# Kernel optimization log

Hardware: AMD Instinct MI355X
Metric: run time of the kernel (lower is better)

The kernel has to match this reference:

```python
import jax, jax.numpy as jnp
import numpy as np

BN_EPS = 1e-5

def _conv1x1(x, w, b):
    # x: [B,C,H,W], w: [O,C], b: [O]
    return jnp.einsum('bchw,oc->bohw', x, w) + b[None, :, None, None]

def _maxpool2x2(x):
    B, C, H, W = x.shape
    return x.reshape(B, C, H // 2, 2, W // 2, 2).max(axis=(3, 5))

def setup_inputs() -> dict:
    key = jax.random.key(0)
    ks = jax.random.split(key, 6)
    B, C, H, W = 8, 256, 64, 64
    Ci = C // 2  # inter_channels default
    x = jax.random.normal(ks[0], (B, C, H, W), jnp.float32)
    s = lambda k, sh: jax.random.normal(k, sh, jnp.float32) * 0.02
    return {
        'x': x,
        'w_g': s(ks[1], (Ci, C)), 'b_g': jnp.zeros((Ci,), jnp.float32),
        'w_theta': s(ks[2], (Ci, C)), 'b_theta': jnp.zeros((Ci,), jnp.float32),
        'w_phi': s(ks[3], (Ci, C)), 'b_phi': jnp.zeros((Ci,), jnp.float32),
        'w_w': s(ks[4], (C, Ci)), 'b_w': jnp.zeros((C,), jnp.float32),
        'bn_gamma': 1.0 + 0.1 * jax.random.normal(ks[5], (C,), jnp.float32),
        'bn_beta': jnp.zeros((C,), jnp.float32),
    }

def reference(x, w_g, b_g, w_theta, b_theta, w_phi, b_phi, w_w, b_w, bn_gamma, bn_beta):
    B, C, H, W = x.shape
    Ci = w_g.shape[0]
    # projections (sub_sample=True: maxpool 2x2 on g and phi)
    g_x = _maxpool2x2(_conv1x1(x, w_g, b_g)).reshape(B, Ci, -1)          # [B,Ci,M]
    g_x = g_x.transpose(0, 2, 1)                                          # [B,M,Ci]
    theta_x = _conv1x1(x, w_theta, b_theta).reshape(B, Ci, -1)            # [B,Ci,N]
    theta_x = theta_x.transpose(0, 2, 1)                                  # [B,N,Ci]
    phi_x = _maxpool2x2(_conv1x1(x, w_phi, b_phi)).reshape(B, Ci, -1)     # [B,Ci,M]
    # unscaled embedded-Gaussian attention (no 1/sqrt(d), as in source)
    f = jnp.einsum('bnc,bcm->bnm', theta_x, phi_x)                        # [B,N,M]
    f_div_C = jax.nn.softmax(f, axis=-1)
    y = jnp.einsum('bnm,bmc->bnc', f_div_C, g_x)                          # [B,N,Ci]
    y = y.transpose(0, 2, 1).reshape(B, Ci, H, W)
    # W: 1x1 conv + BatchNorm (training mode: batch statistics)
    wy = _conv1x1(y, w_w, b_w)                                            # [B,C,H,W]
    mean = wy.mean(axis=(0, 2, 3), keepdims=True)
    var = wy.var(axis=(0, 2, 3), keepdims=True)
    wy = (wy - mean) * jax.lax.rsqrt(var + BN_EPS)
    wy = wy * bn_gamma[None, :, None, None] + bn_beta[None, :, None, None]
    return wy + x
```

## Files before the change

### kernel.cpp

```cpp
#include <hip/hip_runtime.h>
#include <hip/hip_bf16.h>

#define NB 8
#define NC 256
#define NCI 128
#define NSP 4096
#define NM 1024

typedef float f32x4 __attribute__((ext_vector_type(4)));
typedef short s16x8 __attribute__((ext_vector_type(8)));
typedef unsigned short u16;

#define OFF_XH  (0ull)
#define OFF_XL  (16777216ull)
#define OFF_THT (33554432ull)
#define OFF_PHT (41943040ull)
#define OFF_GP  (44040192ull)
#define OFF_YH  (46137344ull)
#define OFF_YL  (54525952ull)
#define OFF_WY  (0ull)
#define OFF_WBH (62914560ull)
#define OFF_WBL (63111168ull)
#define OFF_WWH (63307776ull)
#define OFF_WWL (63373312ull)
#define OFF_S   (63438848ull)

#define GLL(src, dst) __builtin_amdgcn_global_load_lds( \
    (const __attribute__((address_space(1))) unsigned*)(src), \
    (__attribute__((address_space(3))) unsigned*)(dst), 16, 0, 0)

__device__ __forceinline__ u16 f2bf(float f) {
  union { __hip_bfloat16 h; u16 u; } v;
  v.h = __float2bfloat16(f);
  return v.u;
}
__device__ __forceinline__ float bf2f(u16 u) {
  union { unsigned u; float f; } v;
  v.u = (unsigned)u << 16;
  return v.f;
}
__device__ __forceinline__ u16 bfmax4(u16 a, u16 b, u16 c, u16 d) {
  float v = fmaxf(fmaxf(bf2f(a), bf2f(b)), fmaxf(bf2f(c), bf2f(d)));
  return f2bf(v);
}

__global__ void zero_stats(float* s) { s[threadIdx.x] = 0.f; }

__global__ __launch_bounds__(256) void wcvt(
    const float* __restrict__ wg, const float* __restrict__ wth,
    const float* __restrict__ wph, const float* __restrict__ ww,
    u16* __restrict__ wbh, u16* __restrict__ wbl,
    u16* __restrict__ wwh, u16* __restrict__ wwl)
{
  int idx = blockIdx.x * 256 + threadIdx.x;
  if (idx < 384 * 256) {
    int row = idx >> 8, k = idx & 255;
    float v = row < 128 ? wg[row * 256 + k]
            : row < 256 ? wth[(row - 128) * 256 + k]
                        : wph[(row - 256) * 256 + k];
    u16 h = f2bf(v);
    wbh[idx] = h;
    wbl[idx] = f2bf(v - bf2f(h));
  } else {
    int j = idx - 384 * 256;
    float v = ww[j];
    u16 h = f2bf(v);
    wwh[j] = h;
    wwl[j] = f2bf(v - bf2f(h));
  }
}

__global__ __launch_bounds__(256) void xt_cvt(const float* __restrict__ x,
                                              u16* __restrict__ xh, u16* __restrict__ xl)
{
  __shared__ float t[64 * 68];
  const int n0 = blockIdx.x << 6, c0 = blockIdx.y << 6, b = blockIdx.z;
  const int tid = threadIdx.x;
  const int cl = tid >> 4, n4 = (tid & 15) << 2;
#pragma unroll
  for (int it = 0; it < 4; ++it) {
    int c = it * 16 + cl;
    float4 v = *(const float4*)&x[((size_t)(b * NC + c0 + c)) * NSP + n0 + n4];
    *(float4*)&t[c * 68 + n4] = v;
  }
  __syncthreads();
#pragma unroll
  for (int it = 0; it < 2; ++it) {
    int task = it * 256 + tid;
    int n = task >> 3, cc = (task & 7) << 3;
    u16 oh[8], ol[8];
#pragma unroll
    for (int i = 0; i < 8; ++i) {
      float v = t[(cc + i) * 68 + n];
      oh[i] = f2bf(v);
      ol[i] = f2bf(v - bf2f(oh[i]));
    }
    size_t dst = ((size_t)(b * NSP + n0 + n)) * NC + c0 + cc;
    *(s16x8*)&xh[dst] = *(s16x8*)oh;
    *(s16x8*)&xl[dst] = *(s16x8*)ol;
  }
}

__global__ __launch_bounds__(512, 1) void proj_fused(
    const u16* __restrict__ xh, const u16* __restrict__ xl,
    const u16* __restrict__ wbh, const u16* __restrict__ wbl,
    const float* __restrict__ bg, const float* __restrict__ bth,
    const float* __restrict__ bph,
    u16* __restrict__ thT, u16* __restrict__ phT, u16* __restrict__ gp)
{
  __shared__ char smem[132608];
  u16* xsh = (u16*)smem;
  u16* xsl = (u16*)(smem + 16384);
  u16* wsh = (u16*)(smem + 32768);
  u16* wsl = (u16*)(smem + 81920);
  u16* outl = (u16*)smem;
  float* bias = (float*)(smem + 131072);

  const int b = blockIdx.y, h2 = blockIdx.x;
  const int n0 = h2 << 7;
  const int tid = threadIdx.x;
  const int wave = tid >> 6, lane = tid & 63;
  const int lo16 = lane & 15, hi4 = lane >> 4;
  const int wr = wave >> 1, wc = wave & 1;
  const int obase = wr * 96, nbase = wc * 64;

  if (tid < 384)
    bias[tid] = tid < 128 ? bg[tid] : tid < 256 ? bth[tid - 128] : bph[tid - 256];

  f32x4 acc[6][4];
#pragma unroll
  for (int i = 0; i < 6; ++i)
#pragma unroll
    for (int j = 0; j < 4; ++j) acc[i][j] = (f32x4){0.f, 0.f, 0.f, 0.f};

  for (int step = 0; step < 4; ++step) {
    __syncthreads();
#pragma unroll
    for (int i = 0; i < 2; ++i) {
      int ci = i * 512 + tid;
      int n = ci >> 3, slot = ci & 7;
      size_t rowb = ((size_t)(b * NSP + n0 + n)) * 512 + step * 128 + ((slot ^ (n & 7)) << 4);
      GLL((const char*)xh + rowb, (char*)xsh + (size_t)(i * 512 + (tid & ~63)) * 16);
      GLL((const char*)xl + rowb, (char*)xsl + (size_t)(i * 512 + (tid & ~63)) * 16);
    }
#pragma unroll
    for (int i = 0; i < 6; ++i) {
      int ci = i * 512 + tid;
      int o = ci >> 3, slot = ci & 7;
      size_t rowb = (size_t)o * 512 + step * 128 + ((slot ^ (o & 7)) << 4);
      GLL((const char*)wbh + rowb, (char*)wsh + (size_t)(i * 512 + (tid & ~63)) * 16);
      GLL((const char*)wbl + rowb, (char*)wsl + (size_t)(i * 512 + (tid & ~63)) * 16);
    }
    __syncthreads();

#pragma unroll
    for (int kc = 0; kc < 2; ++kc) {
      const int sl = kc * 4 + hi4;
      s16x8 bfh[4], bfl[4];
#pragma unroll
      for (int fn = 0; fn < 4; ++fn) {
        int n = nbase + fn * 16 + lo16;
        int off = (int)n * 128 + ((sl ^ (n & 7)) << 4);
        bfh[fn] = *(const s16x8*)((const char*)xsh + off);
        bfl[fn] = *(const s16x8*)((const char*)xsl + off);
      }
      __builtin_amdgcn_s_setprio(1);
#pragma unroll
      for (int fo = 0; fo < 6; ++fo) {
        int o = obase + fo * 16 + lo16;
        int off = (int)o * 128 + ((sl ^ (o & 7)) << 4);
        s16x8 afh = *(const s16x8*)((const char*)wsh + off);
        s16x8 afl = *(const s16x8*)((const char*)wsl + off);
#pragma unroll
        for (int fn = 0; fn < 4; ++fn) {
          acc[fo][fn] = __builtin_amdgcn_mfma_f32_16x16x32_bf16(afh, bfh[fn], acc[fo][fn], 0, 0, 0);
          acc[fo][fn] = __builtin_amdgcn_mfma_f32_16x16x32_bf16(afh, bfl[fn], acc[fo][fn], 0, 0, 0);
          acc[fo][fn] = __builtin_amdgcn_mfma_f32_16x16x32_bf16(afl, bfh[fn], acc[fo][fn], 0, 0, 0);
        }
      }
      __builtin_amdgcn_s_setprio(0);
    }
  }

  __syncthreads();
#pragma unroll
  for (int fo = 0; fo < 6; ++fo) {
    int orow = obase + fo * 16 + hi4 * 4;
    f32x4 bv = *(const f32x4*)&bias[orow];
#pragma unroll
    for (int fn = 0; fn < 4; ++fn) {
      int n = nbase + fn * 16 + lo16;
#pragma unroll
      for (int r = 0; r < 4; ++r)
        outl[(orow + r) * 137 + n] = f2bf(acc[fo][fn][r] + bv[r]);
    }
  }
  __syncthreads();

#pragma unroll
  for (int it = 0; it < 4; ++it) {
    int task = it * 512 + tid;
    int n = task >> 4, cc = (task & 15) << 3;
    u16 o[8];
#pragma unroll
    for (int i = 0; i < 8; ++i) o[i] = outl[(128 + cc + i) * 137 + n];
    *(s16x8*)&thT[((size_t)(b * NSP + n0 + n)) * NCI + cc] = *(s16x8*)o;
  }
  {
    int c = tid >> 2, wq = tid & 3;
    u16 o[8];
#pragma unroll
    for (int j = 0; j < 8; ++j) {
      int w2 = wq * 8 + j;
      o[j] = bfmax4(outl[c * 137 + 2 * w2], outl[c * 137 + 2 * w2 + 1],
                    outl[c * 137 + 64 + 2 * w2], outl[c * 137 + 64 + 2 * w2 + 1]);
    }
    *(s16x8*)&gp[((size_t)(b * NCI + c)) * NM + (h2 << 5) + wq * 8] = *(s16x8*)o;
  }
  {
    int w2 = tid >> 4, cc = (tid & 15) << 3;
    u16 o[8];
#pragma unroll
    for (int i = 0; i < 8; ++i) {
      int c = 256 + cc + i;
      o[i] = bfmax4(outl[c * 137 + 2 * w2], outl[c * 137 + 2 * w2 + 1],
                    outl[c * 137 + 64 + 2 * w2], outl[c * 137 + 64 + 2 * w2 + 1]);
    }
    *(s16x8*)&phT[((size_t)(b * NM + (h2 << 5) + w2)) * NCI + cc] = *(s16x8*)o;
  }
}

__global__ __launch_bounds__(256, 2) void attn_mfma(
    const u16* __restrict__ thT, const u16* __restrict__ phT,
    const u16* __restrict__ gP, u16* __restrict__ yh, u16* __restrict__ yl)
{
  __shared__ u16 phs[2][64 * 128];
  __shared__ u16 gs[2][128 * 64];
  __shared__ u16 ps[4][16 * 72];

  const int b = blockIdx.y;
  const int n0 = blockIdx.x << 6;
  const int tid = threadIdx.x;
  const int wave = tid >> 6;
  const int lane = tid & 63;
  const int lo16 = lane & 15;
  const int hi4 = lane >> 4;
  const int qbase = n0 + (wave << 4);
  const int swq = (lo16 & 7) << 4;

  s16x8 tha[4];
#pragma unroll
  for (int kc = 0; kc < 4; ++kc)
    tha[kc] = *(const s16x8*)&thT[((size_t)b * NSP + qbase + lo16) * NCI + kc * 32 + hi4 * 8];

  f32x4 yacc[8];
#pragma unroll
  for (int i = 0; i < 8; ++i) yacc[i] = (f32x4){0.f, 0.f, 0.f, 0.f};
  float m_i[4] = {-3e38f, -3e38f, -3e38f, -3e38f};
  float l_i[4] = {0.f, 0.f, 0.f, 0.f};

  auto stage = [&](int s, int m0) {
#pragma unroll
    for (int i = 0; i < 4; ++i) {
      int ci = i * 256 + tid;
      int m = ci >> 4, cb = (ci & 15) << 4;
      const char* src = (const char*)phT + (((size_t)b * NM + m0 + m) << 8) + (cb ^ ((m & 7) << 4));
      GLL(src, (char*)phs[s] + (size_t)(i * 256 + (tid & ~63)) * 16);
    }
#pragma unroll
    for (int i = 0; i < 4; ++i) {
      int ci = i * 256 + tid;
      int c = ci >> 3, mb = (ci & 7) << 4;
      const char* src = (const char*)gP + (((size_t)b * NCI + c) << 11) + m0 * 2 + (mb ^ ((c & 7) << 4));
      GLL(src, (char*)gs[s] + (size_t)(i * 256 + (tid & ~63)) * 16);
    }
  };

  stage(0, 0);
  __syncthreads();
  int cur = 0;

  for (int mt = 0; mt < 16; ++mt) {
    if (mt < 15) stage(cur ^ 1, (mt + 1) << 6);

    const u16* ph = phs[cur];
    const u16* gg = gs[cur];

    f32x4 sf[4];
#pragma unroll
    for (int ms = 0; ms < 4; ++ms) sf[ms] = (f32x4){0.f, 0.f, 0.f, 0.f};
    __builtin_amdgcn_s_setprio(1);
#pragma unroll
    for (int ms = 0; ms < 4; ++ms) {
      const int rbase = (ms * 16 + lo16) << 8;
#pragma unroll
      for (int kc = 0; kc < 4; ++kc) {
        s16x8 bp = *(const s16x8*)((const char*)ph + rbase + ((kc * 64 + hi4 * 16) ^ swq));
        sf[ms] = __builtin_amdgcn_mfma_f32_16x16x32_bf16(tha[kc], bp, sf[ms], 0, 0, 0);
      }
    }
    __builtin_amdgcn_s_setprio(0);

    float scv[4];
#pragma unroll
    for (int r = 0; r < 4; ++r) {
      float v = fmaxf(fmaxf(sf[0][r], sf[1][r]), fmaxf(sf[2][r], sf[3][r]));
      v = fmaxf(v, __shfl_xor(v, 1));
      v = fmaxf(v, __shfl_xor(v, 2));
      v = fmaxf(v, __shfl_xor(v, 4));
      v = fmaxf(v, __shfl_xor(v, 8));
      float mn = fmaxf(m_i[r], v);
      float sc = __expf(m_i[r] - mn);
      float rs = 0.f;
#pragma unroll
      for (int ms = 0; ms < 4; ++ms) {
        float e = __expf(sf[ms][r] - mn);
        sf[ms][r] = e;
        rs += e;
      }
      rs += __shfl_xor(rs, 1);
      rs += __shfl_xor(rs, 2);
      rs += __shfl_xor(rs, 4);
      rs += __shfl_xor(rs, 8);
      l_i[r] = l_i[r] * sc + rs;
      m_i[r] = mn;
      scv[r] = sc;
    }
#pragma unroll
    for (int ct = 0; ct < 8; ++ct)
#pragma unroll
      for (int r = 0; r < 4; ++r) yacc[ct][r] *= scv[r];

    u16* pw = ps[wave];
#pragma unroll
    for (int ms = 0; ms < 4; ++ms)
#pragma unroll
      for (int r = 0; r < 4; ++r)
        pw[(hi4 * 4 + r) * 72 + ms * 16 + lo16] = f2bf(sf[ms][r]);
    asm volatile("s_waitcnt lgkmcnt(0)" ::: "memory");

    s16x8 pa[2];
#pragma unroll
    for (int km = 0; km < 2; ++km)
      pa[km] = *(const s16x8*)((const char*)pw + lo16 * 144 + km * 64 + hi4 * 16);

    __builtin_amdgcn_s_setprio(1);
#pragma unroll
    for (int ct = 0; ct < 8; ++ct) {
      const int rb = (ct * 16 + lo16) << 7;
#pragma unroll
      for (int km = 0; km < 2; ++km) {
        s16x8 bg = *(const s16x8*)((const char*)gg + rb + ((km * 64 + hi4 * 16) ^ swq));
        yacc[ct] = __builtin_amdgcn_mfma_f32_16x16x32_bf16(pa[km], bg, yacc[ct], 0, 0, 0);
      }
    }
    __builtin_amdgcn_s_setprio(0);

    __syncthreads();
    cur ^= 1;
  }

#pragma unroll
  for (int r = 0; r < 4; ++r) {
    float inv = 1.f / l_i[r];
    size_t row = ((size_t)b * NSP + qbase + hi4 * 4 + r) * NCI;
#pragma unroll
    for (int ct = 0; ct < 8; ++ct) {
      float v = yacc[ct][r] * inv;
      u16 h = f2bf(v);
      yh[row + ct * 16 + lo16] = h;
      yl[row + ct * 16 + lo16] = f2bf(v - bf2f(h));
    }
  }
}

__global__ __launch_bounds__(512, 1) void conv_w_mfma(
    const u16* __restrict__ yh, const u16* __restrict__ yl,
    const u16* __restrict__ wwh, const u16* __restrict__ wwl,
    const float* __restrict__ bw, float* __restrict__ wy,
    float* __restrict__ s1g, float* __restrict__ s2g)
{
  __shared__ char smem[102400];
  u16* wsh = (u16*)smem;
  u16* wsl = (u16*)(smem + 32768);
  u16* ysh = (u16*)(smem + 65536);
  u16* ysl = (u16*)(smem + 81920);
  float (*sums1)[256] = (float(*)[256])(smem + 98304);
  float (*sums2)[256] = (float(*)[256])(smem + 100352);

  const int b = blockIdx.y, n0 = blockIdx.x << 7;
  const int tid = threadIdx.x;
  const int wave = tid >> 6, lane = tid & 63;
  const int lo16 = lane & 15, hi4 = lane >> 4;
  const int wr = wave >> 1, wc = wave & 1;
  const int obase = wr * 64, nbase = wc * 64;

  f32x4 acc[4][4];
#pragma unroll
  for (int i = 0; i < 4; ++i)
#pragma unroll
    for (int j = 0; j < 4; ++j) acc[i][j] = (f32x4){0.f, 0.f, 0.f, 0.f};

  for (int step = 0; step < 2; ++step) {
    __syncthreads();
#pragma unroll
    for (int i = 0; i < 4; ++i) {
      int ci = i * 512 + tid;
      int o = ci >> 3, slot = ci & 7;
      size_t rowb = (size_t)o * 256 + step * 128 + ((slot ^ (o & 7)) << 4);
      GLL((const char*)wwh + rowb, (char*)wsh + (size_t)(i * 512 + (tid & ~63)) * 16);
      GLL((const char*)wwl + rowb, (char*)wsl + (size_t)(i * 512 + (tid & ~63)) * 16);
    }
#pragma unroll
    for (int i = 0; i < 2; ++i) {
      int ci = i * 512 + tid;
      int n = ci >> 3, slot = ci & 7;
      size_t rowb = ((size_t)(b * NSP + n0 + n)) * 256 + step * 128 + ((slot ^ (n & 7)) << 4);
      GLL((const char*)yh + rowb, (char*)ysh + (size_t)(i * 512 + (tid & ~63)) * 16);
      GLL((const char*)yl + rowb, (char*)ysl + (size_t)(i * 512 + (tid & ~63)) * 16);
    }
    __syncthreads();

#pragma unroll
    for (int kc = 0; kc < 2; ++kc) {
      const int sl = kc * 4 + hi4;
      s16x8 bfh[4], bfl[4];
#pragma unroll
      for (int fn = 0; fn < 4; ++fn) {
        int n = nbase + fn * 16 + lo16;
        int off = (int)n * 128 + ((sl ^ (n & 7)) << 4);
        bfh[fn] = *(const s16x8*)((const char*)ysh + off);
        bfl[fn] = *(const s16x8*)((const char*)ysl + off);
      }
      __builtin_amdgcn_s_setprio(1);
#pragma unroll
      for (int fo = 0; fo < 4; ++fo) {
        int o = obase + fo * 16 + lo16;
        int off = (int)o * 128 + ((sl ^ (o & 7)) << 4);
        s16x8 afh = *(const s16x8*)((const char*)wsh + off);
        s16x8 afl = *(const s16x8*)((const char*)wsl + off);
#pragma unroll
        for (int fn = 0; fn < 4; ++fn) {
          acc[fo][fn] = __builtin_amdgcn_mfma_f32_16x16x32_bf16(afh, bfh[fn], acc[fo][fn], 0, 0, 0);
          acc[fo][fn] = __builtin_amdgcn_mfma_f32_16x16x32_bf16(afh, bfl[fn], acc[fo][fn], 0, 0, 0);
          acc[fo][fn] = __builtin_amdgcn_mfma_f32_16x16x32_bf16(afl, bfh[fn], acc[fo][fn], 0, 0, 0);
        }
      }
      __builtin_amdgcn_s_setprio(0);
    }
  }

#pragma unroll
  for (int fo = 0; fo < 4; ++fo) {
    int orow = obase + fo * 16 + hi4 * 4;
    float bv[4];
#pragma unroll
    for (int r = 0; r < 4; ++r) bv[r] = bw[orow + r];
    float ss[4] = {0.f, 0.f, 0.f, 0.f}, sq[4] = {0.f, 0.f, 0.f, 0.f};
#pragma unroll
    for (int fn = 0; fn < 4; ++fn) {
      int col = n0 + nbase + fn * 16 + lo16;
#pragma unroll
      for (int r = 0; r < 4; ++r) {
        float v = acc[fo][fn][r] + bv[r];
        wy[((size_t)(b * NC) + orow + r) * NSP + col] = v;
        ss[r] += v;
        sq[r] += v * v;
      }
    }
#pragma unroll
    for (int r = 0; r < 4; ++r) {
#pragma unroll
      for (int d = 1; d < 16; d <<= 1) {
        ss[r] += __shfl_xor(ss[r], d);
        sq[r] += __shfl_xor(sq[r], d);
      }
    }
    if (lo16 == 0) {
#pragma unroll
      for (int r = 0; r < 4; ++r) {
        sums1[wc][orow + r] = ss[r];
        sums2[wc][orow + r] = sq[r];
      }
    }
  }
  __syncthreads();
  if (tid < 256) {
    atomicAdd(&s1g[tid], sums1[0][tid] + sums1[1][tid]);
    atomicAdd(&s2g[tid], sums2[0][tid] + sums2[1][tid]);
  }
}

__global__ __launch_bounds__(256) void bn_res4(
    const float* __restrict__ wy, const float* __restrict__ x,
    const float* __restrict__ s1, const float* __restrict__ s2,
    const float* __restrict__ gamma, const float* __restrict__ beta,
    float* __restrict__ out)
{
  int i4 = (blockIdx.x * 256 + threadIdx.x) << 2;
  int c = (i4 >> 12) & 255;
  const float cnt = 1.f / 32768.f;
  float mean = s1[c] * cnt;
  float var = s2[c] * cnt - mean * mean;
  float inv = rsqrtf(var + 1e-5f) * gamma[c];
  float bet = beta[c];
  float4 w = *(const float4*)&wy[i4];
  float4 xv = *(const float4*)&x[i4];
  float4 o;
  o.x = (w.x - mean) * inv + bet + xv.x;
  o.y = (w.y - mean) * inv + bet + xv.y;
  o.z = (w.z - mean) * inv + bet + xv.z;
  o.w = (w.w - mean) * inv + bet + xv.w;
  *(float4*)&out[i4] = o;
}

extern "C" void kernel_launch(void* const* d_in, const int* in_sizes, int n_in,
                              void* d_out, int out_size, void* d_ws, size_t ws_size,
                              hipStream_t stream) {
  const float* x    = (const float*)d_in[0];
  const float* w_g  = (const float*)d_in[1];
  const float* b_g  = (const float*)d_in[2];
  const float* w_th = (const float*)d_in[3];
  const float* b_th = (const float*)d_in[4];
  const float* w_ph = (const float*)d_in[5];
  const float* b_ph = (const float*)d_in[6];
  const float* w_w  = (const float*)d_in[7];
  const float* b_w  = (const float*)d_in[8];
  const float* gam  = (const float*)d_in[9];
  const float* bet  = (const float*)d_in[10];
  float* out = (float*)d_out;
  char* ws = (char*)d_ws;

  u16*   xh  = (u16*)(ws + OFF_XH);
  u16*   xl  = (u16*)(ws + OFF_XL);
  u16*   thT = (u16*)(ws + OFF_THT);
  u16*   phT = (u16*)(ws + OFF_PHT);
  u16*   gp  = (u16*)(ws + OFF_GP);
  u16*   yhb = (u16*)(ws + OFF_YH);
  u16*   ylb = (u16*)(ws + OFF_YL);
  float* wy  = (float*)(ws + OFF_WY);
  u16*   wbh = (u16*)(ws + OFF_WBH);
  u16*   wbl = (u16*)(ws + OFF_WBL);
  u16*   wwh = (u16*)(ws + OFF_WWH);
  u16*   wwl = (u16*)(ws + OFF_WWL);
  float* s1  = (float*)(ws + OFF_S);
  float* s2  = s1 + 256;

  wcvt<<<dim3(512), 256, 0, stream>>>(w_g, w_th, w_ph, w_w, wbh, wbl, wwh, wwl);
  zero_stats<<<dim3(1), 512, 0, stream>>>(s1);
  xt_cvt<<<dim3(64, 4, 8), 256, 0, stream>>>(x, xh, xl);

  proj_fused<<<dim3(32, 8), 512, 0, stream>>>(xh, xl, wbh, wbl, b_g, b_th, b_ph, thT, phT, gp);

  attn_mfma<<<dim3(64, 8), 256, 0, stream>>>(thT, phT, gp, yhb, ylb);

  conv_w_mfma<<<dim3(32, 8), 512, 0, stream>>>(yhb, ylb, wwh, wwl, b_w, wy, s1, s2);

  bn_res4<<<dim3(8192), 256, 0, stream>>>(wy, x, s1, s2, gam, bet, out);
}
```

Before: 125.7 us.

## Rewrite attention with 32x32x16 MFMA, transposed scores, register-resident P

Switches the attention kernel from 16x16x32 to 32x32x16 bf16 MFMA. Each wave now handles 32 queries and each block 128 queries, so the grid is halved. Scores are computed transposed so each lane owns one query row, which turns the softmax max and sum reductions into in-register loops plus one cross-half shuffle. The probability operand is built with packed bf16 conversion and permlane32 swaps instead of a trip through shared memory. Output is written through an LDS bounce buffer for coalesced 16-byte stores. In exchange, only 256 blocks run with a single block per CU, which cuts occupancy and latency hiding on a 256-CU part.

```diff
diff --git a/kernel.cpp b/kernel.cpp
--- a/kernel.cpp
+++ b/kernel.cpp
@@ -8,6 +8,7 @@
 #define NM 1024
 
 typedef float f32x4 __attribute__((ext_vector_type(4)));
+typedef float f32x16 __attribute__((ext_vector_type(16)));
 typedef short s16x8 __attribute__((ext_vector_type(8)));
 typedef unsigned short u16;
 
@@ -42,6 +43,11 @@
 __device__ __forceinline__ u16 bfmax4(u16 a, u16 b, u16 c, u16 d) {
   float v = fmaxf(fmaxf(bf2f(a), bf2f(b)), fmaxf(bf2f(c), bf2f(d)));
   return f2bf(v);
+}
+__device__ __forceinline__ unsigned cvtpk(float lo, float hi) {
+  unsigned r;
+  asm volatile("v_cvt_pk_bf16_f32 %0, %1, %2" : "=v"(r) : "v"(lo), "v"(hi));
+  return r;
 }
 
 __global__ void zero_stats(float* s) { s[threadIdx.x] = 0.f; }
@@ -230,49 +236,50 @@
   }
 }
 
-__global__ __launch_bounds__(256, 2) void attn_mfma(
+__global__ __launch_bounds__(256, 1) void attn_mfma(
     const u16* __restrict__ thT, const u16* __restrict__ phT,
     const u16* __restrict__ gP, u16* __restrict__ yh, u16* __restrict__ yl)
 {
-  __shared__ u16 phs[2][64 * 128];
-  __shared__ u16 gs[2][128 * 64];
-  __shared__ u16 ps[4][16 * 72];
+  __shared__ char smem[65536];
 
   const int b = blockIdx.y;
-  const int n0 = blockIdx.x << 6;
+  const int n0 = blockIdx.x << 7;
   const int tid = threadIdx.x;
   const int wave = tid >> 6;
   const int lane = tid & 63;
-  const int lo16 = lane & 15;
-  const int hi4 = lane >> 4;
-  const int qbase = n0 + (wave << 4);
-  const int swq = (lo16 & 7) << 4;
-
-  s16x8 tha[4];
-#pragma unroll
-  for (int kc = 0; kc < 4; ++kc)
-    tha[kc] = *(const s16x8*)&thT[((size_t)b * NSP + qbase + lo16) * NCI + kc * 32 + hi4 * 8];
-
-  f32x4 yacc[8];
-#pragma unroll
-  for (int i = 0; i < 8; ++i) yacc[i] = (f32x4){0.f, 0.f, 0.f, 0.f};
-  float m_i[4] = {-3e38f, -3e38f, -3e38f, -3e38f};
-  float l_i[4] = {0.f, 0.f, 0.f, 0.f};
+  const int l31 = lane & 31;
+  const int hi1 = lane >> 5;
+  const int qbase = n0 + (wave << 5);
+  const int swl = (l31 & 7) << 4;
+
+  s16x8 thb[8];
+  {
+    const u16* tr = &thT[((size_t)b * NSP + qbase + l31) * NCI + hi1 * 8];
+#pragma unroll
+    for (int kc = 0; kc < 8; ++kc) thb[kc] = *(const s16x8*)&tr[kc * 16];
+  }
+
+  f32x16 yacc[4];
+#pragma unroll
+  for (int ct = 0; ct < 4; ++ct) yacc[ct] = (f32x16)0.f;
+  float m_i = -3e38f, l_i = 0.f;
 
   auto stage = [&](int s, int m0) {
+    char* pdst = smem + s * 16384;
+    char* gdst = smem + 32768 + s * 16384;
 #pragma unroll
     for (int i = 0; i < 4; ++i) {
       int ci = i * 256 + tid;
       int m = ci >> 4, cb = (ci & 15) << 4;
       const char* src = (const char*)phT + (((size_t)b * NM + m0 + m) << 8) + (cb ^ ((m & 7) << 4));
-      GLL(src, (char*)phs[s] + (size_t)(i * 256 + (tid & ~63)) * 16);
+      GLL(src, pdst + (size_t)(i * 256 + (tid & ~63)) * 16);
     }
 #pragma unroll
     for (int i = 0; i < 4; ++i) {
       int ci = i * 256 + tid;
       int c = ci >> 3, mb = (ci & 7) << 4;
       const char* src = (const char*)gP + (((size_t)b * NCI + c) << 11) + m0 * 2 + (mb ^ ((c & 7) << 4));
-      GLL(src, (char*)gs[s] + (size_t)(i * 256 + (tid & ~63)) * 16);
+      GLL(src, gdst + (size_t)(i * 256 + (tid & ~63)) * 16);
     }
   };
 
@@ -282,76 +289,72 @@
 
   for (int mt = 0; mt < 16; ++mt) {
     if (mt < 15) stage(cur ^ 1, (mt + 1) << 6);
-
-    const u16* ph = phs[cur];
-    const u16* gg = gs[cur];
-
-    f32x4 sf[4];
-#pragma unroll
-    for (int ms = 0; ms < 4; ++ms) sf[ms] = (f32x4){0.f, 0.f, 0.f, 0.f};
+    const char* ph = smem + cur * 16384;
+    const char* gg = smem + 32768 + cur * 16384;
+
+    f32x16 s0 = (f32x16)0.f, s1 = (f32x16)0.f;
     __builtin_amdgcn_s_setprio(1);
 #pragma unroll
-    for (int ms = 0; ms < 4; ++ms) {
-      const int rbase = (ms * 16 + lo16) << 8;
-#pragma unroll
-      for (int kc = 0; kc < 4; ++kc) {
-        s16x8 bp = *(const s16x8*)((const char*)ph + rbase + ((kc * 64 + hi4 * 16) ^ swq));
-        sf[ms] = __builtin_amdgcn_mfma_f32_16x16x32_bf16(tha[kc], bp, sf[ms], 0, 0, 0);
-      }
+    for (int kc = 0; kc < 8; ++kc) {
+      int cofs = (kc * 32 + hi1 * 16);
+      s16x8 a0 = *(const s16x8*)(ph + l31 * 256 + (cofs ^ swl));
+      s16x8 a1 = *(const s16x8*)(ph + (32 + l31) * 256 + (cofs ^ swl));
+      s0 = __builtin_amdgcn_mfma_f32_32x32x16_bf16(a0, thb[kc], s0, 0, 0, 0);
+      s1 = __builtin_amdgcn_mfma_f32_32x32x16_bf16(a1, thb[kc], s1, 0, 0, 0);
     }
     __builtin_amdgcn_s_setprio(0);
 
-    float scv[4];
-#pragma unroll
-    for (int r = 0; r < 4; ++r) {
-      float v = fmaxf(fmaxf(sf[0][r], sf[1][r]), fmaxf(sf[2][r], sf[3][r]));
-      v = fmaxf(v, __shfl_xor(v, 1));
-      v = fmaxf(v, __shfl_xor(v, 2));
-      v = fmaxf(v, __shfl_xor(v, 4));
-      v = fmaxf(v, __shfl_xor(v, 8));
-      float mn = fmaxf(m_i[r], v);
-      float sc = __expf(m_i[r] - mn);
-      float rs = 0.f;
-#pragma unroll
-      for (int ms = 0; ms < 4; ++ms) {
-        float e = __expf(sf[ms][r] - mn);
-        sf[ms][r] = e;
-        rs += e;
-      }
-      rs += __shfl_xor(rs, 1);
-      rs += __shfl_xor(rs, 2);
-      rs += __shfl_xor(rs, 4);
-      rs += __shfl_xor(rs, 8);
-      l_i[r] = l_i[r] * sc + rs;
-      m_i[r] = mn;
-      scv[r] = sc;
-    }
-#pragma unroll
-    for (int ct = 0; ct < 8; ++ct)
-#pragma unroll
-      for (int r = 0; r < 4; ++r) yacc[ct][r] *= scv[r];
-
-    u16* pw = ps[wave];
-#pragma unroll
-    for (int ms = 0; ms < 4; ++ms)
-#pragma unroll
-      for (int r = 0; r < 4; ++r)
-        pw[(hi4 * 4 + r) * 72 + ms * 16 + lo16] = f2bf(sf[ms][r]);
-    asm volatile("s_waitcnt lgkmcnt(0)" ::: "memory");
-
-    s16x8 pa[2];
-#pragma unroll
-    for (int km = 0; km < 2; ++km)
-      pa[km] = *(const s16x8*)((const char*)pw + lo16 * 144 + km * 64 + hi4 * 16);
+    float pm = s0[0];
+#pragma unroll
+    for (int i = 1; i < 16; ++i) pm = fmaxf(pm, s0[i]);
+#pragma unroll
+    for (int i = 0; i < 16; ++i) pm = fmaxf(pm, s1[i]);
+    pm = fmaxf(pm, __shfl_xor(pm, 32));
+    float mn = fmaxf(m_i, pm);
+    float sc = __expf(m_i - mn);
+    float rs = 0.f;
+#pragma unroll
+    for (int i = 0; i < 16; ++i) { s0[i] = __expf(s0[i] - mn); rs += s0[i]; }
+#pragma unroll
+    for (int i = 0; i < 16; ++i) { s1[i] = __expf(s1[i] - mn); rs += s1[i]; }
+    rs += __shfl_xor(rs, 32);
+    l_i = l_i * sc + rs;
+    m_i = mn;
+#pragma unroll
+    for (int ct = 0; ct < 4; ++ct)
+#pragma unroll
+      for (int i = 0; i < 16; ++i) yacc[ct][i] *= sc;
+
+    s16x8 pb[4];
+#pragma unroll
+    for (int km = 0; km < 4; ++km) {
+      int r0 = (km & 1) * 8;
+      unsigned X0, X1, X2, X3;
+      if (km < 2) {
+        X0 = cvtpk(s0[r0 + 0], s0[r0 + 1]);
+        X1 = cvtpk(s0[r0 + 2], s0[r0 + 3]);
+        X2 = cvtpk(s0[r0 + 4], s0[r0 + 5]);
+        X3 = cvtpk(s0[r0 + 6], s0[r0 + 7]);
+      } else {
+        X0 = cvtpk(s1[r0 + 0], s1[r0 + 1]);
+        X1 = cvtpk(s1[r0 + 2], s1[r0 + 3]);
+        X2 = cvtpk(s1[r0 + 4], s1[r0 + 5]);
+        X3 = cvtpk(s1[r0 + 6], s1[r0 + 7]);
+      }
+      asm volatile("v_permlane32_swap_b32 %0, %1" : "+v"(X0), "+v"(X2));
+      asm volatile("v_permlane32_swap_b32 %0, %1" : "+v"(X1), "+v"(X3));
+      unsigned d[4] = {X0, X1, X2, X3};
+      pb[km] = *(s16x8*)d;
+    }
 
     __builtin_amdgcn_s_setprio(1);
 #pragma unroll
-    for (int ct = 0; ct < 8; ++ct) {
-      const int rb = (ct * 16 + lo16) << 7;
-#pragma unroll
-      for (int km = 0; km < 2; ++km) {
-        s16x8 bg = *(const s16x8*)((const char*)gg + rb + ((km * 64 + hi4 * 16) ^ swq));
-        yacc[ct] = __builtin_amdgcn_mfma_f32_16x16x32_bf16(pa[km], bg, yacc[ct], 0, 0, 0);
+    for (int ct = 0; ct < 4; ++ct) {
+      const char* grow = gg + (ct * 32 + l31) * 128;
+#pragma unroll
+      for (int km = 0; km < 4; ++km) {
+        s16x8 ga = *(const s16x8*)(grow + ((km * 32 + hi1 * 16) ^ swl));
+        yacc[ct] = __builtin_amdgcn_mfma_f32_32x32x16_bf16(ga, pb[km], yacc[ct], 0, 0, 0);
       }
     }
     __builtin_amdgcn_s_setprio(0);
@@ -360,17 +363,36 @@
     cur ^= 1;
   }
 
-#pragma unroll
-  for (int r = 0; r < 4; ++r) {
-    float inv = 1.f / l_i[r];
-    size_t row = ((size_t)b * NSP + qbase + hi4 * 4 + r) * NCI;
-#pragma unroll
-    for (int ct = 0; ct < 8; ++ct) {
-      float v = yacc[ct][r] * inv;
-      u16 h = f2bf(v);
-      yh[row + ct * 16 + lo16] = h;
-      yl[row + ct * 16 + lo16] = f2bf(v - bf2f(h));
-    }
+  float inv = 1.f / l_i;
+#pragma unroll
+  for (int ct = 0; ct < 4; ++ct)
+#pragma unroll
+    for (int i = 0; i < 16; ++i) yacc[ct][i] *= inv;
+
+  u16* bounce = (u16*)smem;
+  const int qq = lane >> 1, c0 = (lane & 1) << 6;
+#pragma unroll
+  for (int pass = 0; pass < 2; ++pass) {
+    __syncthreads();
+#pragma unroll
+    for (int ct = 0; ct < 4; ++ct) {
+#pragma unroll
+      for (int rp = 0; rp < 8; ++rp) {
+        int r = rp * 2;
+        int c = ct * 32 + (r & 3) + 8 * (r >> 2) + 4 * hi1;
+        float v0 = yacc[ct][r], v1 = yacc[ct][r + 1];
+        u16 h0 = f2bf(v0), h1 = f2bf(v1);
+        u16 w0 = h0, w1 = h1;
+        if (pass) { w0 = f2bf(v0 - bf2f(h0)); w1 = f2bf(v1 - bf2f(h1)); }
+        *(unsigned*)&bounce[wave * 4224 + l31 * 132 + c] = (unsigned)w0 | ((unsigned)w1 << 16);
+      }
+    }
+    __syncthreads();
+    u16* dst = pass ? yl : yh;
+    size_t row = ((size_t)b * NSP + qbase + qq) * NCI + c0;
+#pragma unroll
+    for (int k = 0; k < 8; ++k)
+      *(s16x8*)&dst[row + k * 8] = *(const s16x8*)&bounce[wave * 4224 + qq * 132 + c0 + k * 8];
   }
 }
 
@@ -552,7 +574,7 @@
 
   proj_fused<<<dim3(32, 8), 512, 0, stream>>>(xh, xl, wbh, wbl, b_g, b_th, b_ph, thT, phT, gp);
 
-  attn_mfma<<<dim3(64, 8), 256, 0, stream>>>(thT, phT, gp, yhb, ylb);
+  attn_mfma<<<dim3(32, 8), 256, 0, stream>>>(thT, phT, gp, yhb, ylb);
 
   conv_w_mfma<<<dim3(32, 8), 512, 0, stream>>>(yhb, ylb, wwh, wwl, b_w, wy, s1, s2);
 
```

Result: faster. 119.6 us (-4.9%).
